# Kernel optimization log

Measured on AMD Instinct MI355X. Metric: run time of the kernel, lower is better.

Reference implementation:

```python
import jax, jax.numpy as jnp
import numpy as np

jax.config.update("jax_enable_x64", True)

# --- static config (matches init_kwargs) ---
L = 6            # voxel_level_num
F = 8            # feature_dim
T = 524288       # per-level feature table size
B = 4194304      # buffer_size (hash table size)
N = 1048576      # number of query points
LEAF = 0.25      # leaf_voxel_size
UP = 2.0         # up_scale_factor

PRIMES = jnp.array([73856093, 19349669, 83492791], dtype=jnp.int64)
# corner offsets, z varies fastest (same order as torch self.steps)
STEPS = jnp.array([[0,0,0],[0,0,1],[0,1,0],[0,1,1],
                   [1,0,0],[1,0,1],[1,1,0],[1,1,1]], dtype=jnp.float32)


def setup_inputs() -> dict:
    key = jax.random.key(0)
    k1, k2, k3, k4 = jax.random.split(key, 4)
    query_points = jax.random.uniform(k1, (N, 3), dtype=jnp.float32) * 50.0
    features = 0.01 * jax.random.normal(k2, (L, T, F), dtype=jnp.float32)
    idx = jax.random.randint(k3, (L, B), 0, T, dtype=jnp.int64)
    empty = jax.random.uniform(k4, (L, B)) < 0.2
    feature_indexs = jnp.where(empty, jnp.int64(-1), idx)
    return {"query_points": query_points, "features": features,
            "feature_indexs": feature_indexs}


def _trilinear_coeffs(d):
    # d: [N,3] fractional coords in the cell; order matches STEPS (z fastest)
    tx, ty, tz = d[:, 0], d[:, 1], d[:, 2]
    return jnp.stack([
        (1-tx)*(1-ty)*(1-tz), (1-tx)*(1-ty)*tz,
        (1-tx)*ty*(1-tz),     (1-tx)*ty*tz,
        tx*(1-ty)*(1-tz),     tx*(1-ty)*tz,
        tx*ty*(1-tz),         tx*ty*tz,
    ], axis=1)  # [N,8]


def reference(query_points, features, feature_indexs):
    out = jnp.zeros((query_points.shape[0], F), dtype=query_points.dtype)
    for i in range(L):  # small fixed level loop (structurally distinct resolutions)
        res = LEAF * (UP ** i)
        scaled = query_points / res                      # [N,3]
        base = jnp.floor(scaled)
        corners = (base[:, None, :] + STEPS[None]).astype(jnp.int64)  # [N,8,3]
        keys = jnp.mod((corners * PRIMES).sum(-1), B)    # [N,8] spatial hash
        idx = feature_indexs[i][keys]                    # [N,8] gather, -1 = empty
        valid = idx.min(axis=1) > -1                     # [N] all 8 corners allocated
        coeffs = _trilinear_coeffs(scaled - base)        # [N,8]
        feats = features[i][jnp.clip(idx, 0, T - 1)]     # [N,8,F] gather
        level = jnp.einsum('nkf,nk->nf', feats, coeffs)  # trilinear interp
        out = out + jnp.where(valid[:, None], level, jnp.zeros((), out.dtype))
    return out
```

## Files before the change

kernel.cpp:

```cpp
#include <hip/hip_runtime.h>


static constexpr int      NPTS  = 1048576;
static constexpr int      LVLS  = 6;
static constexpr int      NF    = 8;
static constexpr int      TTAB  = 524288;
static constexpr unsigned BTAB  = 4194304u;
static constexpr unsigned BMASK = BTAB - 1u;
static constexpr unsigned P0 = 73856093u, P1 = 19349669u, P2 = 83492791u;

static constexpr int NBIN = 4096;
static constexpr int SB   = 256;
static constexpr int PPB  = NPTS / SB;
static constexpr int ITER = PPB / 256;
static constexpr int BCAP = 512;

static constexpr int    BMW_L        = BTAB / 32;
static constexpr size_t SORTED_BYTES = (size_t)NPTS * 16;
static constexpr size_t BM_BYTES     = (size_t)LVLS * BMW_L * 4;

typedef float f4 __attribute__((ext_vector_type(4)));
typedef int   i4 __attribute__((ext_vector_type(4)));

__global__ __launch_bounds__(256) void bmbuild_k(const int* __restrict__ fidx,
                                                 unsigned* __restrict__ bm) {
    const int g = blockIdx.x * 256 + threadIdx.x;
    const i4* p = (const i4*)(fidx + (size_t)g * 32);
    unsigned w = 0;
#pragma unroll
    for (int j = 0; j < 8; ++j) {
        const i4 v = __builtin_nontemporal_load(p + j);
        w |= (unsigned)(v.x >= 0) << (4 * j + 0);
        w |= (unsigned)(v.y >= 0) << (4 * j + 1);
        w |= (unsigned)(v.z >= 0) << (4 * j + 2);
        w |= (unsigned)(v.w >= 0) << (4 * j + 3);
    }
    bm[g] = w;
}

__device__ __forceinline__ void nhv_point_bm(
    float qx, float qy, float qz,
    const float* __restrict__ feat, const int* __restrict__ fidx,
    const unsigned* __restrict__ bm, float acc[NF])
{
    float    fx[LVLS], fy[LVLS], fz[LVLS];
    unsigned h[LVLS];
#pragma unroll
    for (int i = 0; i < LVLS; ++i) {
        const float inv = 4.0f / (float)(1 << i);
        const float sx = qx * inv, sy = qy * inv, sz = qz * inv;
        const float bx = floorf(sx), by = floorf(sy), bz = floorf(sz);
        fx[i] = sx - bx; fy[i] = sy - by; fz[i] = sz - bz;
        h[i] = (unsigned)(int)bx * P0 + (unsigned)(int)by * P1 + (unsigned)(int)bz * P2;
    }

    unsigned vmask = 0;
#pragma unroll
    for (int i = 0; i < LVLS; ++i) {
        const unsigned* __restrict__ bl = bm + i * BMW_L;
        unsigned v = ~0u;
#pragma unroll
        for (int k = 0; k < 8; ++k) {
            unsigned key = h[i];
            if (k & 4) key += P0;
            if (k & 2) key += P1;
            if (k & 1) key += P2;
            key &= BMASK;
            v &= (bl[key >> 5] >> (key & 31u));
        }
        vmask |= (v & 1u) << i;
    }

#pragma unroll
    for (int f = 0; f < NF; ++f) acc[f] = 0.0f;

#pragma unroll
    for (int i = 0; i < LVLS; ++i) {
        if (vmask & (1u << i)) {
            const int* __restrict__ tab = fidx + (size_t)i * BTAB;
            int id[8];
#pragma unroll
            for (int k = 0; k < 8; ++k) {
                unsigned key = h[i];
                if (k & 4) key += P0;
                if (k & 2) key += P1;
                if (k & 1) key += P2;
                id[k] = tab[key & BMASK];
            }
            const float wxv[2] = {1.0f - fx[i], fx[i]};
            const float wyv[2] = {1.0f - fy[i], fy[i]};
            const float wzv[2] = {1.0f - fz[i], fz[i]};
            const float* __restrict__ fb = feat + (size_t)i * (TTAB * NF);
#pragma unroll
            for (int k = 0; k < 8; ++k) {
                const float c = wxv[(k >> 2) & 1] * wyv[(k >> 1) & 1] * wzv[k & 1];
                const float4* p = (const float4*)(fb + (size_t)id[k] * NF);
                const float4 lo = p[0];
                const float4 hi = p[1];
                acc[0] += c * lo.x; acc[1] += c * lo.y;
                acc[2] += c * lo.z; acc[3] += c * lo.w;
                acc[4] += c * hi.x; acc[5] += c * hi.y;
                acc[6] += c * hi.z; acc[7] += c * hi.w;
            }
        }
    }
}

__device__ __forceinline__ void nhv_point(
    float qx, float qy, float qz,
    const float* __restrict__ feat, const int* __restrict__ fidx, float acc[NF])
{
    float    fx[LVLS], fy[LVLS], fz[LVLS];
    unsigned h[LVLS];
#pragma unroll
    for (int i = 0; i < LVLS; ++i) {
        const float inv = 4.0f / (float)(1 << i);
        const float sx = qx * inv, sy = qy * inv, sz = qz * inv;
        const float bx = floorf(sx), by = floorf(sy), bz = floorf(sz);
        fx[i] = sx - bx; fy[i] = sy - by; fz[i] = sz - bz;
        h[i] = (unsigned)(int)bx * P0 + (unsigned)(int)by * P1 + (unsigned)(int)bz * P2;
    }
    int id[LVLS][8];
#pragma unroll
    for (int i = 0; i < LVLS; ++i) {
        const int* __restrict__ tab = fidx + (size_t)i * BTAB;
#pragma unroll
        for (int k = 0; k < 8; ++k) {
            unsigned key = h[i];
            if (k & 4) key += P0;
            if (k & 2) key += P1;
            if (k & 1) key += P2;
            id[i][k] = tab[key & BMASK];
        }
    }
#pragma unroll
    for (int f = 0; f < NF; ++f) acc[f] = 0.0f;
#pragma unroll
    for (int i = 0; i < LVLS; ++i) {
        int mn = id[i][0];
#pragma unroll
        for (int k = 1; k < 8; ++k) mn = min(mn, id[i][k]);
        if (mn > -1) {
            const float wxv[2] = {1.0f - fx[i], fx[i]};
            const float wyv[2] = {1.0f - fy[i], fy[i]};
            const float wzv[2] = {1.0f - fz[i], fz[i]};
            const float* __restrict__ fb = feat + (size_t)i * (TTAB * NF);
#pragma unroll
            for (int k = 0; k < 8; ++k) {
                const float c = wxv[(k >> 2) & 1] * wyv[(k >> 1) & 1] * wzv[k & 1];
                const float4* p = (const float4*)(fb + (size_t)id[i][k] * NF);
                const float4 lo = p[0];
                const float4 hi = p[1];
                acc[0] += c * lo.x; acc[1] += c * lo.y;
                acc[2] += c * lo.z; acc[3] += c * lo.w;
                acc[4] += c * hi.x; acc[5] += c * hi.y;
                acc[6] += c * hi.z; acc[7] += c * hi.w;
            }
        }
    }
}

__device__ __forceinline__ unsigned expand4(unsigned v) {
    return (v & 1u) | ((v & 2u) << 2) | ((v & 4u) << 4) | ((v & 8u) << 6);
}
__device__ __forceinline__ unsigned bin_of(float x, float y, float z) {
    unsigned bx = min(15u, (unsigned)(int)(x * 0.32f));
    unsigned by = min(15u, (unsigned)(int)(y * 0.32f));
    unsigned bz = min(15u, (unsigned)(int)(z * 0.32f));
    return expand4(bx) | (expand4(by) << 1) | (expand4(bz) << 2);
}

__global__ __launch_bounds__(256) void hist_k(const float* __restrict__ qp,
                                              unsigned* __restrict__ hist) {
    __shared__ unsigned lh[NBIN];
    const int b = blockIdx.x, t = threadIdx.x;
    for (int i = t; i < NBIN; i += 256) lh[i] = 0u;
    __syncthreads();
    const int base = b * PPB;
#pragma unroll
    for (int i = 0; i < ITER; ++i) {
        const int p = base + i * 256 + t;
        atomicAdd(&lh[bin_of(qp[3*p], qp[3*p+1], qp[3*p+2])], 1u);
    }
    __syncthreads();
    for (int i = t; i < NBIN; i += 256) hist[(size_t)b * NBIN + i] = lh[i];
}

__global__ __launch_bounds__(256) void colscan_k(unsigned* __restrict__ hist,
                                                 unsigned* __restrict__ binbase) {
    const int bin = blockIdx.x * 256 + threadIdx.x;
    unsigned run = 0;
    for (int b = 0; b < SB; ++b) {
        const unsigned v = hist[(size_t)b * NBIN + bin];
        hist[(size_t)b * NBIN + bin] = run;
        run += v;
    }
    binbase[bin] = run;
}

__global__ __launch_bounds__(256) void binscan_k(unsigned* __restrict__ binbase) {
    __shared__ unsigned tot[256];
    const int t = threadIdx.x;
    unsigned v[16];
    unsigned s = 0;
#pragma unroll
    for (int i = 0; i < 16; ++i) { v[i] = s; s += binbase[t * 16 + i]; }
    tot[t] = s;
    __syncthreads();
    for (int d = 1; d < 256; d <<= 1) {
        const unsigned x = (t >= d) ? tot[t - d] : 0u;
        __syncthreads();
        tot[t] += x;
        __syncthreads();
    }
    const unsigned cb = tot[t] - s;
#pragma unroll
    for (int i = 0; i < 16; ++i) binbase[t * 16 + i] = cb + v[i];
}

__global__ __launch_bounds__(256) void scatter_k(const float* __restrict__ qp,
                                                 const unsigned* __restrict__ hist,
                                                 const unsigned* __restrict__ binbase,
                                                 float4* __restrict__ sorted) {
    __shared__ unsigned cur[NBIN];
    const int b = blockIdx.x, t = threadIdx.x;
    for (int i = t; i < NBIN; i += 256)
        cur[i] = binbase[i] + hist[(size_t)b * NBIN + i];
    __syncthreads();
    const int base = b * PPB;
#pragma unroll
    for (int i = 0; i < ITER; ++i) {
        const int p = base + i * 256 + t;
        const float x = qp[3*p], y = qp[3*p+1], z = qp[3*p+2];
        const unsigned slot = atomicAdd(&cur[bin_of(x, y, z)], 1u);
        sorted[slot] = make_float4(x, y, z, __uint_as_float((unsigned)p));
    }
}

__global__ __launch_bounds__(256) void binsort_k(float4* __restrict__ sorted,
                                                 const unsigned* __restrict__ binbase) {
    __shared__ float4        pts[BCAP];
    __shared__ unsigned char sk[BCAP];
    __shared__ unsigned      cnt[64];

    const int bin = blockIdx.x, t = threadIdx.x;
    const unsigned start = binbase[bin];
    const unsigned end   = (bin < NBIN - 1) ? binbase[bin + 1] : (unsigned)NPTS;
    const int n = (int)(end - start);
    if (n <= 1 || n > BCAP) return;

    if (t < 64) cnt[t] = 0u;
    __syncthreads();
#pragma unroll
    for (int r = 0; r < BCAP / 256; ++r) {
        const int i = r * 256 + t;
        if (i < n) {
            const float4 p = sorted[start + i];
            pts[i] = p;
            const unsigned ux = (unsigned)(int)(p.x * 1.28f) & 3u;
            const unsigned uy = (unsigned)(int)(p.y * 1.28f) & 3u;
            const unsigned uz = (unsigned)(int)(p.z * 1.28f) & 3u;
            const unsigned s = (ux & 1u) | ((uy & 1u) << 1) | ((uz & 1u) << 2)
                             | ((ux >> 1) << 3) | ((uy >> 1) << 4) | ((uz >> 1) << 5);
            sk[i] = (unsigned char)s;
            atomicAdd(&cnt[s], 1u);
        }
    }
    __syncthreads();
    if (t == 0) {
        unsigned run = 0;
#pragma unroll
        for (int i = 0; i < 64; ++i) { const unsigned v = cnt[i]; cnt[i] = run; run += v; }
    }
    __syncthreads();
#pragma unroll
    for (int r = 0; r < BCAP / 256; ++r) {
        const int i = r * 256 + t;
        if (i < n) {
            const unsigned dest = atomicAdd(&cnt[sk[i]], 1u);
            sorted[start + dest] = pts[i];
        }
    }
}

__global__ __launch_bounds__(256) void nhv_sorted_bm_k(
    const float4* __restrict__ sp, const float* __restrict__ feat,
    const int* __restrict__ fidx, const unsigned* __restrict__ bm,
    float* __restrict__ out)
{
    const int nwg = NPTS / 256;
    const int bid = blockIdx.x;
    const int swz = (bid & 7) * (nwg >> 3) + (bid >> 3);
    const int j   = swz * 256 + (int)threadIdx.x;

    const f4 s = __builtin_nontemporal_load((const f4*)sp + j);
    float acc[NF];
    nhv_point_bm(s.x, s.y, s.z, feat, fidx, bm, acc);
    const unsigned n = __float_as_uint(s.w);

    f4* o = (f4*)(out + (size_t)n * NF);
    f4 lo = {acc[0], acc[1], acc[2], acc[3]};
    f4 hi = {acc[4], acc[5], acc[6], acc[7]};
    __builtin_nontemporal_store(lo, o);
    __builtin_nontemporal_store(hi, o + 1);
}

__global__ __launch_bounds__(256) void nhv_sorted_k(
    const float4* __restrict__ sp, const float* __restrict__ feat,
    const int* __restrict__ fidx, float* __restrict__ out)
{
    const int nwg = NPTS / 256;
    const int bid = blockIdx.x;
    const int swz = (bid & 7) * (nwg >> 3) + (bid >> 3);
    const int j   = swz * 256 + (int)threadIdx.x;

    const f4 s = __builtin_nontemporal_load((const f4*)sp + j);
    float acc[NF];
    nhv_point(s.x, s.y, s.z, feat, fidx, acc);
    const unsigned n = __float_as_uint(s.w);
    f4* o = (f4*)(out + (size_t)n * NF);
    f4 lo = {acc[0], acc[1], acc[2], acc[3]};
    f4 hi = {acc[4], acc[5], acc[6], acc[7]};
    __builtin_nontemporal_store(lo, o);
    __builtin_nontemporal_store(hi, o + 1);
}

__global__ __launch_bounds__(256) void nhv_direct_k(
    const float* __restrict__ qp, const float* __restrict__ feat,
    const int* __restrict__ fidx, float* __restrict__ out)
{
    const int n = blockIdx.x * 256 + threadIdx.x;
    if (n >= NPTS) return;
    float acc[NF];
    nhv_point(qp[3*n], qp[3*n+1], qp[3*n+2], feat, fidx, acc);
    float4* o = (float4*)(out + (size_t)n * NF);
    o[0] = make_float4(acc[0], acc[1], acc[2], acc[3]);
    o[1] = make_float4(acc[4], acc[5], acc[6], acc[7]);
}

extern "C" void kernel_launch(void* const* d_in, const int* in_sizes, int n_in,
                              void* d_out, int out_size, void* d_ws, size_t ws_size,
                              hipStream_t stream) {
    const float* qp   = (const float*)d_in[0];
    const float* feat = (const float*)d_in[1];
    const int*   fidx = (const int*)d_in[2];
    float*       out  = (float*)d_out;

    unsigned* hist    = (unsigned*)d_out;
    unsigned* binbase = hist + (size_t)SB * NBIN;

    if (ws_size >= SORTED_BYTES + BM_BYTES) {
        float4*   sorted = (float4*)d_ws;
        unsigned* bm     = (unsigned*)((char*)d_ws + SORTED_BYTES);

        hipLaunchKernelGGL(bmbuild_k, dim3(LVLS * BMW_L / 256), dim3(256), 0, stream, fidx, bm);
        hipLaunchKernelGGL(hist_k,    dim3(SB),   dim3(256), 0, stream, qp, hist);
        hipLaunchKernelGGL(colscan_k, dim3(16),   dim3(256), 0, stream, hist, binbase);
        hipLaunchKernelGGL(binscan_k, dim3(1),    dim3(256), 0, stream, binbase);
        hipLaunchKernelGGL(scatter_k, dim3(SB),   dim3(256), 0, stream, qp, hist, binbase, sorted);
        hipLaunchKernelGGL(binsort_k, dim3(NBIN), dim3(256), 0, stream, sorted, binbase);
        hipLaunchKernelGGL(nhv_sorted_bm_k, dim3(NPTS/256), dim3(256), 0, stream,
                           sorted, feat, fidx, bm, out);
    } else if (ws_size >= SORTED_BYTES) {
        float4* sorted = (float4*)d_ws;
        hipLaunchKernelGGL(hist_k,    dim3(SB),   dim3(256), 0, stream, qp, hist);
        hipLaunchKernelGGL(colscan_k, dim3(16),   dim3(256), 0, stream, hist, binbase);
        hipLaunchKernelGGL(binscan_k, dim3(1),    dim3(256), 0, stream, binbase);
        hipLaunchKernelGGL(scatter_k, dim3(SB),   dim3(256), 0, stream, qp, hist, binbase, sorted);
        hipLaunchKernelGGL(binsort_k, dim3(NBIN), dim3(256), 0, stream, sorted, binbase);
        hipLaunchKernelGGL(nhv_sorted_k, dim3(NPTS/256), dim3(256), 0, stream,
                           sorted, feat, fidx, out);
    } else {
        hipLaunchKernelGGL(nhv_direct_k, dim3(NPTS/256), dim3(256), 0, stream,
                           qp, feat, fidx, out);
    }
}
```

Before: 229.8 us.

## Fuse bitmap build with histogram and bin sort with interpolation kernel

Merges the bitmap-building kernel and histogram kernel into one launch, and fuses the per-bin sub-sort into the main interpolation kernel so points are reordered in shared memory and processed directly, without writing back to global memory. The main kernel now runs one workgroup per bin, with launch bounds requesting higher occupancy. Per-level hash and fraction values are recomputed rather than kept live, to reduce register pressure. In exchange, per-bin workgroups carry uneven work, and there are extra shared-memory syncs before compute.

```diff
diff --git a/kernel.cpp b/kernel.cpp
--- a/kernel.cpp
+++ b/kernel.cpp
@@ -16,59 +16,46 @@
 static constexpr int BCAP = 512;
 
 static constexpr int    BMW_L        = BTAB / 32;
+static constexpr int    BM_BLOCKS    = LVLS * BMW_L / 256;
 static constexpr size_t SORTED_BYTES = (size_t)NPTS * 16;
 static constexpr size_t BM_BYTES     = (size_t)LVLS * BMW_L * 4;
+static constexpr size_t BB_BYTES     = (size_t)NBIN * 4;
+static constexpr size_t WS_FULL      = SORTED_BYTES + BM_BYTES + BB_BYTES;
 
 typedef float f4 __attribute__((ext_vector_type(4)));
 typedef int   i4 __attribute__((ext_vector_type(4)));
-
-__global__ __launch_bounds__(256) void bmbuild_k(const int* __restrict__ fidx,
-                                                 unsigned* __restrict__ bm) {
-    const int g = blockIdx.x * 256 + threadIdx.x;
-    const i4* p = (const i4*)(fidx + (size_t)g * 32);
-    unsigned w = 0;
-#pragma unroll
-    for (int j = 0; j < 8; ++j) {
-        const i4 v = __builtin_nontemporal_load(p + j);
-        w |= (unsigned)(v.x >= 0) << (4 * j + 0);
-        w |= (unsigned)(v.y >= 0) << (4 * j + 1);
-        w |= (unsigned)(v.z >= 0) << (4 * j + 2);
-        w |= (unsigned)(v.w >= 0) << (4 * j + 3);
-    }
-    bm[g] = w;
-}
 
 __device__ __forceinline__ void nhv_point_bm(
     float qx, float qy, float qz,
     const float* __restrict__ feat, const int* __restrict__ fidx,
     const unsigned* __restrict__ bm, float acc[NF])
 {
-    float    fx[LVLS], fy[LVLS], fz[LVLS];
-    unsigned h[LVLS];
-#pragma unroll
-    for (int i = 0; i < LVLS; ++i) {
-        const float inv = 4.0f / (float)(1 << i);
-        const float sx = qx * inv, sy = qy * inv, sz = qz * inv;
-        const float bx = floorf(sx), by = floorf(sy), bz = floorf(sz);
-        fx[i] = sx - bx; fy[i] = sy - by; fz[i] = sz - bz;
-        h[i] = (unsigned)(int)bx * P0 + (unsigned)(int)by * P1 + (unsigned)(int)bz * P2;
-    }
-
     unsigned vmask = 0;
 #pragma unroll
-    for (int i = 0; i < LVLS; ++i) {
-        const unsigned* __restrict__ bl = bm + i * BMW_L;
-        unsigned v = ~0u;
-#pragma unroll
-        for (int k = 0; k < 8; ++k) {
-            unsigned key = h[i];
-            if (k & 4) key += P0;
-            if (k & 2) key += P1;
-            if (k & 1) key += P2;
-            key &= BMASK;
-            v &= (bl[key >> 5] >> (key & 31u));
-        }
-        vmask |= (v & 1u) << i;
+    for (int half = 0; half < 2; ++half) {
+        unsigned hh[3];
+#pragma unroll
+        for (int j = 0; j < 3; ++j) {
+            const int i = half * 3 + j;
+            const float inv = 4.0f / (float)(1 << i);
+            const float bx = floorf(qx * inv), by = floorf(qy * inv), bz = floorf(qz * inv);
+            hh[j] = (unsigned)(int)bx * P0 + (unsigned)(int)by * P1 + (unsigned)(int)bz * P2;
+        }
+#pragma unroll
+        for (int j = 0; j < 3; ++j) {
+            const unsigned* __restrict__ bl = bm + (size_t)(half * 3 + j) * BMW_L;
+            unsigned vv = ~0u;
+#pragma unroll
+            for (int k = 0; k < 8; ++k) {
+                unsigned key = hh[j];
+                if (k & 4) key += P0;
+                if (k & 2) key += P1;
+                if (k & 1) key += P2;
+                key &= BMASK;
+                vv &= (bl[key >> 5] >> (key & 31u));
+            }
+            vmask |= (vv & 1u) << (half * 3 + j);
+        }
     }
 
 #pragma unroll
@@ -77,19 +64,25 @@
 #pragma unroll
     for (int i = 0; i < LVLS; ++i) {
         if (vmask & (1u << i)) {
+            const float inv = 4.0f / (float)(1 << i);
+            const float sx = qx * inv, sy = qy * inv, sz = qz * inv;
+            const float bx = floorf(sx), by = floorf(sy), bz = floorf(sz);
+            const unsigned h = (unsigned)(int)bx * P0 + (unsigned)(int)by * P1
+                             + (unsigned)(int)bz * P2;
             const int* __restrict__ tab = fidx + (size_t)i * BTAB;
             int id[8];
 #pragma unroll
             for (int k = 0; k < 8; ++k) {
-                unsigned key = h[i];
+                unsigned key = h;
                 if (k & 4) key += P0;
                 if (k & 2) key += P1;
                 if (k & 1) key += P2;
                 id[k] = tab[key & BMASK];
             }
-            const float wxv[2] = {1.0f - fx[i], fx[i]};
-            const float wyv[2] = {1.0f - fy[i], fy[i]};
-            const float wzv[2] = {1.0f - fz[i], fz[i]};
+            const float tx = sx - bx, ty = sy - by, tz = sz - bz;
+            const float wxv[2] = {1.0f - tx, tx};
+            const float wyv[2] = {1.0f - ty, ty};
+            const float wzv[2] = {1.0f - tz, tz};
             const float* __restrict__ fb = feat + (size_t)i * (TTAB * NF);
 #pragma unroll
             for (int k = 0; k < 8; ++k) {
@@ -170,20 +163,38 @@
     return expand4(bx) | (expand4(by) << 1) | (expand4(bz) << 2);
 }
 
-__global__ __launch_bounds__(256) void hist_k(const float* __restrict__ qp,
-                                              unsigned* __restrict__ hist) {
+__global__ __launch_bounds__(256) void pre_k(const int* __restrict__ fidx,
+                                             unsigned* __restrict__ bm,
+                                             const float* __restrict__ qp,
+                                             unsigned* __restrict__ hist) {
     __shared__ unsigned lh[NBIN];
-    const int b = blockIdx.x, t = threadIdx.x;
-    for (int i = t; i < NBIN; i += 256) lh[i] = 0u;
-    __syncthreads();
-    const int base = b * PPB;
-#pragma unroll
-    for (int i = 0; i < ITER; ++i) {
-        const int p = base + i * 256 + t;
-        atomicAdd(&lh[bin_of(qp[3*p], qp[3*p+1], qp[3*p+2])], 1u);
-    }
-    __syncthreads();
-    for (int i = t; i < NBIN; i += 256) hist[(size_t)b * NBIN + i] = lh[i];
+    const int t = threadIdx.x;
+    if (blockIdx.x < BM_BLOCKS) {
+        const int g = blockIdx.x * 256 + t;
+        const i4* p = (const i4*)(fidx + (size_t)g * 32);
+        unsigned w = 0;
+#pragma unroll
+        for (int j = 0; j < 8; ++j) {
+            const i4 v = __builtin_nontemporal_load(p + j);
+            w |= (unsigned)(v.x >= 0) << (4 * j + 0);
+            w |= (unsigned)(v.y >= 0) << (4 * j + 1);
+            w |= (unsigned)(v.z >= 0) << (4 * j + 2);
+            w |= (unsigned)(v.w >= 0) << (4 * j + 3);
+        }
+        bm[g] = w;
+    } else {
+        const int b = blockIdx.x - BM_BLOCKS;
+        for (int i = t; i < NBIN; i += 256) lh[i] = 0u;
+        __syncthreads();
+        const int base = b * PPB;
+#pragma unroll
+        for (int i = 0; i < ITER; ++i) {
+            const int p = base + i * 256 + t;
+            atomicAdd(&lh[bin_of(qp[3*p], qp[3*p+1], qp[3*p+2])], 1u);
+        }
+        __syncthreads();
+        for (int i = t; i < NBIN; i += 256) hist[(size_t)b * NBIN + i] = lh[i];
+    }
 }
 
 __global__ __launch_bounds__(256) void colscan_k(unsigned* __restrict__ hist,
@@ -237,92 +248,83 @@
     }
 }
 
-__global__ __launch_bounds__(256) void binsort_k(float4* __restrict__ sorted,
-                                                 const unsigned* __restrict__ binbase) {
-    __shared__ float4        pts[BCAP];
-    __shared__ unsigned char sk[BCAP];
-    __shared__ unsigned      cnt[64];
-
-    const int bin = blockIdx.x, t = threadIdx.x;
+__global__ __launch_bounds__(256, 7) void nhv_main_k(
+    const float4* __restrict__ sorted, const unsigned* __restrict__ binbase,
+    const float* __restrict__ feat, const int* __restrict__ fidx,
+    const unsigned* __restrict__ bm, float* __restrict__ out)
+{
+    __shared__ float4         pts[BCAP];
+    __shared__ unsigned char  sk[BCAP];
+    __shared__ unsigned short ord[BCAP];
+    __shared__ unsigned       cnt[64];
+
+    const int bid = blockIdx.x;
+    const int bin = (bid & 7) * (NBIN >> 3) + (bid >> 3);
+    const int t   = threadIdx.x;
     const unsigned start = binbase[bin];
     const unsigned end   = (bin < NBIN - 1) ? binbase[bin + 1] : (unsigned)NPTS;
     const int n = (int)(end - start);
-    if (n <= 1 || n > BCAP) return;
-
-    if (t < 64) cnt[t] = 0u;
-    __syncthreads();
-#pragma unroll
-    for (int r = 0; r < BCAP / 256; ++r) {
-        const int i = r * 256 + t;
-        if (i < n) {
-            const float4 p = sorted[start + i];
-            pts[i] = p;
-            const unsigned ux = (unsigned)(int)(p.x * 1.28f) & 3u;
-            const unsigned uy = (unsigned)(int)(p.y * 1.28f) & 3u;
-            const unsigned uz = (unsigned)(int)(p.z * 1.28f) & 3u;
-            const unsigned s = (ux & 1u) | ((uy & 1u) << 1) | ((uz & 1u) << 2)
-                             | ((ux >> 1) << 3) | ((uy >> 1) << 4) | ((uz >> 1) << 5);
-            sk[i] = (unsigned char)s;
-            atomicAdd(&cnt[s], 1u);
-        }
-    }
-    __syncthreads();
-    if (t == 0) {
-        unsigned run = 0;
-#pragma unroll
-        for (int i = 0; i < 64; ++i) { const unsigned v = cnt[i]; cnt[i] = run; run += v; }
-    }
-    __syncthreads();
-#pragma unroll
-    for (int r = 0; r < BCAP / 256; ++r) {
-        const int i = r * 256 + t;
-        if (i < n) {
-            const unsigned dest = atomicAdd(&cnt[sk[i]], 1u);
-            sorted[start + dest] = pts[i];
-        }
-    }
-}
-
-__global__ __launch_bounds__(256) void nhv_sorted_bm_k(
-    const float4* __restrict__ sp, const float* __restrict__ feat,
-    const int* __restrict__ fidx, const unsigned* __restrict__ bm,
-    float* __restrict__ out)
-{
-    const int nwg = NPTS / 256;
-    const int bid = blockIdx.x;
-    const int swz = (bid & 7) * (nwg >> 3) + (bid >> 3);
-    const int j   = swz * 256 + (int)threadIdx.x;
-
-    const f4 s = __builtin_nontemporal_load((const f4*)sp + j);
-    float acc[NF];
-    nhv_point_bm(s.x, s.y, s.z, feat, fidx, bm, acc);
-    const unsigned n = __float_as_uint(s.w);
-
-    f4* o = (f4*)(out + (size_t)n * NF);
-    f4 lo = {acc[0], acc[1], acc[2], acc[3]};
-    f4 hi = {acc[4], acc[5], acc[6], acc[7]};
-    __builtin_nontemporal_store(lo, o);
-    __builtin_nontemporal_store(hi, o + 1);
-}
-
-__global__ __launch_bounds__(256) void nhv_sorted_k(
-    const float4* __restrict__ sp, const float* __restrict__ feat,
-    const int* __restrict__ fidx, float* __restrict__ out)
-{
-    const int nwg = NPTS / 256;
-    const int bid = blockIdx.x;
-    const int swz = (bid & 7) * (nwg >> 3) + (bid >> 3);
-    const int j   = swz * 256 + (int)threadIdx.x;
-
-    const f4 s = __builtin_nontemporal_load((const f4*)sp + j);
-    float acc[NF];
-    nhv_point(s.x, s.y, s.z, feat, fidx, acc);
-    const unsigned n = __float_as_uint(s.w);
-    f4* o = (f4*)(out + (size_t)n * NF);
-    f4 lo = {acc[0], acc[1], acc[2], acc[3]};
-    f4 hi = {acc[4], acc[5], acc[6], acc[7]};
-    __builtin_nontemporal_store(lo, o);
-    __builtin_nontemporal_store(hi, o + 1);
+
+    if (n <= BCAP) {
+        if (t < 64) cnt[t] = 0u;
+        __syncthreads();
+#pragma unroll
+        for (int r = 0; r < BCAP / 256; ++r) {
+            const int i = r * 256 + t;
+            if (i < n) {
+                const f4 pv = __builtin_nontemporal_load((const f4*)sorted + (start + i));
+                const float4 p = make_float4(pv.x, pv.y, pv.z, pv.w);
+                pts[i] = p;
+                const unsigned ux = (unsigned)(int)(p.x * 1.28f) & 3u;
+                const unsigned uy = (unsigned)(int)(p.y * 1.28f) & 3u;
+                const unsigned uz = (unsigned)(int)(p.z * 1.28f) & 3u;
+                const unsigned s = (ux & 1u) | ((uy & 1u) << 1) | ((uz & 1u) << 2)
+                                 | ((ux >> 1) << 3) | ((uy >> 1) << 4) | ((uz >> 1) << 5);
+                sk[i] = (unsigned char)s;
+                atomicAdd(&cnt[s], 1u);
+            }
+        }
+        __syncthreads();
+        if (t == 0) {
+            unsigned run = 0;
+#pragma unroll
+            for (int i = 0; i < 64; ++i) { const unsigned v = cnt[i]; cnt[i] = run; run += v; }
+        }
+        __syncthreads();
+#pragma unroll
+        for (int r = 0; r < BCAP / 256; ++r) {
+            const int i = r * 256 + t;
+            if (i < n) ord[atomicAdd(&cnt[sk[i]], 1u)] = (unsigned short)i;
+        }
+        __syncthreads();
+#pragma unroll
+        for (int r = 0; r < BCAP / 256; ++r) {
+            const int j = r * 256 + t;
+            if (j < n) {
+                const float4 p = pts[ord[j]];
+                float acc[NF];
+                nhv_point_bm(p.x, p.y, p.z, feat, fidx, bm, acc);
+                const unsigned pn = __float_as_uint(p.w);
+                f4* o = (f4*)(out + (size_t)pn * NF);
+                f4 lo = {acc[0], acc[1], acc[2], acc[3]};
+                f4 hi = {acc[4], acc[5], acc[6], acc[7]};
+                __builtin_nontemporal_store(lo, o);
+                __builtin_nontemporal_store(hi, o + 1);
+            }
+        }
+    } else {
+        for (int j = t; j < n; j += 256) {
+            const f4 pv = __builtin_nontemporal_load((const f4*)sorted + (start + j));
+            float acc[NF];
+            nhv_point_bm(pv.x, pv.y, pv.z, feat, fidx, bm, acc);
+            const unsigned pn = __float_as_uint(pv.w);
+            f4* o = (f4*)(out + (size_t)pn * NF);
+            f4 lo = {acc[0], acc[1], acc[2], acc[3]};
+            f4 hi = {acc[4], acc[5], acc[6], acc[7]};
+            __builtin_nontemporal_store(lo, o);
+            __builtin_nontemporal_store(hi, o + 1);
+        }
+    }
 }
 
 __global__ __launch_bounds__(256) void nhv_direct_k(
@@ -346,30 +348,19 @@
     const int*   fidx = (const int*)d_in[2];
     float*       out  = (float*)d_out;
 
-    unsigned* hist    = (unsigned*)d_out;
-    unsigned* binbase = hist + (size_t)SB * NBIN;
-
-    if (ws_size >= SORTED_BYTES + BM_BYTES) {
-        float4*   sorted = (float4*)d_ws;
-        unsigned* bm     = (unsigned*)((char*)d_ws + SORTED_BYTES);
-
-        hipLaunchKernelGGL(bmbuild_k, dim3(LVLS * BMW_L / 256), dim3(256), 0, stream, fidx, bm);
-        hipLaunchKernelGGL(hist_k,    dim3(SB),   dim3(256), 0, stream, qp, hist);
-        hipLaunchKernelGGL(colscan_k, dim3(16),   dim3(256), 0, stream, hist, binbase);
-        hipLaunchKernelGGL(binscan_k, dim3(1),    dim3(256), 0, stream, binbase);
-        hipLaunchKernelGGL(scatter_k, dim3(SB),   dim3(256), 0, stream, qp, hist, binbase, sorted);
-        hipLaunchKernelGGL(binsort_k, dim3(NBIN), dim3(256), 0, stream, sorted, binbase);
-        hipLaunchKernelGGL(nhv_sorted_bm_k, dim3(NPTS/256), dim3(256), 0, stream,
-                           sorted, feat, fidx, bm, out);
-    } else if (ws_size >= SORTED_BYTES) {
-        float4* sorted = (float4*)d_ws;
-        hipLaunchKernelGGL(hist_k,    dim3(SB),   dim3(256), 0, stream, qp, hist);
-        hipLaunchKernelGGL(colscan_k, dim3(16),   dim3(256), 0, stream, hist, binbase);
-        hipLaunchKernelGGL(binscan_k, dim3(1),    dim3(256), 0, stream, binbase);
-        hipLaunchKernelGGL(scatter_k, dim3(SB),   dim3(256), 0, stream, qp, hist, binbase, sorted);
-        hipLaunchKernelGGL(binsort_k, dim3(NBIN), dim3(256), 0, stream, sorted, binbase);
-        hipLaunchKernelGGL(nhv_sorted_k, dim3(NPTS/256), dim3(256), 0, stream,
-                           sorted, feat, fidx, out);
+    if (ws_size >= WS_FULL) {
+        float4*   sorted  = (float4*)d_ws;
+        unsigned* bm      = (unsigned*)((char*)d_ws + SORTED_BYTES);
+        unsigned* binbase = (unsigned*)((char*)d_ws + SORTED_BYTES + BM_BYTES);
+        unsigned* hist    = (unsigned*)d_out;
+
+        hipLaunchKernelGGL(pre_k,     dim3(BM_BLOCKS + SB), dim3(256), 0, stream,
+                           fidx, bm, qp, hist);
+        hipLaunchKernelGGL(colscan_k, dim3(16),  dim3(256), 0, stream, hist, binbase);
+        hipLaunchKernelGGL(binscan_k, dim3(1),   dim3(256), 0, stream, binbase);
+        hipLaunchKernelGGL(scatter_k, dim3(SB),  dim3(256), 0, stream, qp, hist, binbase, sorted);
+        hipLaunchKernelGGL(nhv_main_k, dim3(NBIN), dim3(256), 0, stream,
+                           sorted, binbase, feat, fidx, bm, out);
     } else {
         hipLaunchKernelGGL(nhv_direct_k, dim3(NPTS/256), dim3(256), 0, stream,
                            qp, feat, fidx, out);
```

After: 423.9 us. +84.5%, slower.
